# Kernel optimization log

Hardware: AMD Instinct MI355X
Metric: run time of the kernel (lower is better)

## Reference

```python
import jax, jax.numpy as jnp
import numpy as np

N_NODES = 8192
N_EDGES = 262144
FEAT = 128


def _lin(key, fan_in, fan_out):
    k1, k2 = jax.random.split(key)
    s = 1.0 / np.sqrt(fan_in)
    w = jax.random.uniform(k1, (fan_in, fan_out), jnp.float32, -s, s)
    b = jax.random.uniform(k2, (fan_out,), jnp.float32, -s, s)
    return w, b


def setup_inputs() -> dict:
    key = jax.random.key(0)
    ks = jax.random.split(key, 16)
    adj = jax.random.randint(ks[0], (2, N_EDGES), 0, N_NODES)
    features = jax.random.normal(ks[1], (N_NODES, FEAT), jnp.float32)
    w1, b1 = _lin(ks[2], FEAT, 64)
    w2, b2 = _lin(ks[3], 64, 32)
    w3, b3 = _lin(ks[4], 32, 32)
    # MultiheadAttention params (embed_dim=32, 1 head)
    kq = jax.random.split(ks[5], 2)
    wqkv = jax.random.uniform(kq[0], (96, 32), jnp.float32, -1/np.sqrt(32), 1/np.sqrt(32))
    bqkv = jnp.zeros((96,), jnp.float32)
    wo = jax.random.uniform(kq[1], (32, 32), jnp.float32, -1/np.sqrt(32), 1/np.sqrt(32))
    bo = jnp.zeros((32,), jnp.float32)
    w4, b4 = _lin(ks[6], 32, 32)
    w5a, b5a = _lin(ks[7], 32, 32)
    w6a, b6a = _lin(ks[8], 32, 64)
    w7a, b7a = _lin(ks[9], 64, 2)
    w5f, b5f = _lin(ks[10], 32, 32)
    w6f, b6f = _lin(ks[11], 32, 64)
    w7f, b7f = _lin(ks[12], 64, FEAT)
    return dict(adj=adj, features=features, w1=w1, b1=b1, w2=w2, b2=b2, w3=w3, b3=b3,
                wqkv=wqkv, bqkv=bqkv, wo=wo, bo=bo, w4=w4, b4=b4,
                w5a=w5a, b5a=b5a, w6a=w6a, b6a=b6a, w7a=w7a, b7a=b7a,
                w5f=w5f, b5f=b5f, w6f=w6f, b6f=b6f, w7f=w7f, b7f=b7f)


def _gcn(x, w, b, src, dst, norm, n):
    # PyG GCNConv: out = scatter_add(norm * (x W)[src] -> dst) + b
    h = x @ w
    return jax.ops.segment_sum(h[src] * norm[:, None], dst, num_segments=n) + b


def reference(adj, features, w1, b1, w2, b2, w3, b3, wqkv, bqkv, wo, bo, w4, b4,
              w5a, b5a, w6a, b6a, w7a, b7a, w5f, b5f, w6f, b6f, w7f, b7f):
    n = features.shape[0]
    loops = jnp.arange(n)
    src = jnp.concatenate([adj[0], loops])  # self-loops added (gcn_norm)
    dst = jnp.concatenate([adj[1], loops])
    deg = jax.ops.segment_sum(jnp.ones_like(src, jnp.float32), dst, num_segments=n)
    dinv = jnp.where(deg > 0, jax.lax.rsqrt(deg), 0.0)
    norm = dinv[src] * dinv[dst]

    h = jax.nn.relu(_gcn(features, w1, b1, src, dst, norm, n))
    h = jax.nn.relu(_gcn(h, w2, b2, src, dst, norm, n))
    h = jax.nn.relu(_gcn(h, w3, b3, src, dst, norm, n))

    # single-head self-attention over all nodes (seq_len=n, batch=1)
    qkv = h @ wqkv.T + bqkv
    q, k, v = jnp.split(qkv, 3, axis=-1)  # [n,32] each
    attn = jax.nn.softmax((q @ k.T) * (1.0 / np.sqrt(32.0)), axis=-1)  # [n,n]
    h = (attn @ v) @ wo.T + bo

    h = jax.nn.relu(_gcn(h, w4, b4, src, dst, norm, n))

    da = jax.nn.relu(_gcn(h, w5a, b5a, src, dst, norm, n))
    da = jax.nn.relu(_gcn(da, w6a, b6a, src, dst, norm, n))
    da = jax.nn.relu(_gcn(da, w7a, b7a, src, dst, norm, n))  # [n,2]

    df = jax.nn.relu(_gcn(h, w5f, b5f, src, dst, norm, n))
    df = jax.nn.relu(_gcn(df, w6f, b6f, src, dst, norm, n))
    df = jax.nn.relu(_gcn(df, w7f, b7f, src, dst, norm, n))  # [n,FEAT]
    return (da, df)
```

## Files before the change

kernel.cpp:

```cpp
#include <hip/hip_runtime.h>

#define N_NODES 8192
#define N_EDGES 262144

typedef __attribute__((ext_vector_type(4))) float f32x4;
typedef _Float16 half8 __attribute__((ext_vector_type(8)));
typedef _Float16 half4v __attribute__((ext_vector_type(4)));
typedef __fp16 fp16x2 __attribute__((ext_vector_type(2)));
union UH { half8 h8; fp16x2 h2[4]; };
union HC { _Float16 h; unsigned short u; };


__global__ void __launch_bounds__(256) zero_kernel(int4* __restrict__ p) {
  p[blockIdx.x * 256 + threadIdx.x] = make_int4(0, 0, 0, 0);
}


__global__ void __launch_bounds__(1024) scan_kernel(const int* __restrict__ cnt,
                                                    int* __restrict__ rp,
                                                    float* __restrict__ dinv,
                                                    int* __restrict__ cur) {
  __shared__ int sums[1024];
  const int t = threadIdx.x;
  const int base = t * 8;
  int c[8];
  int s = 0;
#pragma unroll
  for (int i = 0; i < 8; ++i) { c[i] = cnt[base + i]; s += c[i]; cur[base + i] = 0; }
  sums[t] = s;
  __syncthreads();
  for (int off = 1; off < 1024; off <<= 1) {
    int v = (t >= off) ? sums[t - off] : 0;
    __syncthreads();
    sums[t] += v;
    __syncthreads();
  }
  int run = (t == 0) ? 0 : sums[t - 1];
#pragma unroll
  for (int i = 0; i < 8; ++i) {
    rp[base + i] = run;
    run += c[i];
    dinv[base + i] = rsqrtf((float)(c[i] + 1));
  }
  if (t == 1023) rp[N_NODES] = run;
}

__global__ void __launch_bounds__(256) fill_kernel(const int* __restrict__ src,
                                                   const int* __restrict__ dst,
                                                   const int* __restrict__ rp,
                                                   const float* __restrict__ dinv,
                                                   int* __restrict__ cur,
                                                   int* __restrict__ col,
                                                   float* __restrict__ wgt) {
  int e = blockIdx.x * 256 + threadIdx.x;
  int d = dst[e], s = src[e];
  int p = atomicAdd(&cur[d], 1);
  int at = rp[d] + p;
  col[at] = s;
  wgt[at] = dinv[s] * dinv[d];
}


template <int FIN, int FOUT, bool WT, bool BIAS, bool RELU, bool O16>
__device__ __forceinline__ void mm_body(const float* __restrict__ x,
                                        const float* __restrict__ w,
                                        const float* __restrict__ bias, void* out,
                                        int bx, int tid, float* ws, float* xs) {
  constexpr int VEC = (FOUT >= 32) ? 4 : 1;
  constexpr int TC = FOUT / VEC;
  constexpr int ROWS = 256 / TC;
  const int r0 = bx * ROWS;
  for (int i = tid; i < FIN * FOUT; i += 256) {
    int k = i / FOUT, j = i % FOUT;
    ws[i] = WT ? w[j * FIN + k] : w[i];
  }
  for (int i = tid; i < ROWS * FIN; i += 256) {
    int r = i / FIN, k = i % FIN;
    xs[r * (FIN + 1) + k] = x[(size_t)(r0 + r) * FIN + k];
  }
  __syncthreads();
  const int jc = tid % TC, r = tid / TC;
  float acc[VEC];
#pragma unroll
  for (int v = 0; v < VEC; ++v) acc[v] = 0.0f;
#pragma unroll
  for (int k = 0; k < FIN; ++k) {
    const float xv = xs[r * (FIN + 1) + k];
#pragma unroll
    for (int v = 0; v < VEC; ++v) acc[v] += xv * ws[k * FOUT + jc * VEC + v];
  }
  float oval[VEC];
#pragma unroll
  for (int v = 0; v < VEC; ++v) {
    int j = jc * VEC + v;
    float o = BIAS ? (acc[v] + bias[j]) : acc[v];
    if (RELU) o = fmaxf(o, 0.0f);
    oval[v] = o;
  }
  if constexpr (O16 && VEC == 4) {
    unsigned short* o16 = (unsigned short*)out;
    half4v pk;
#pragma unroll
    for (int v = 0; v < 4; ++v) pk[v] = (_Float16)oval[v];
    *(half4v*)&o16[(size_t)(r0 + r) * FOUT + jc * 4] = pk;
  } else {
    float* of = (float*)out;
#pragma unroll
    for (int v = 0; v < VEC; ++v) of[(size_t)(r0 + r) * FOUT + jc * VEC + v] = oval[v];
  }
}


template <int FIN, bool I16, bool GBR>
__device__ __forceinline__ void gather_row(const void* __restrict__ t,
                                           const int* __restrict__ rp,
                                           const int* __restrict__ col,
                                           const float* __restrict__ wgt,
                                           const float* __restrict__ dinv,
                                           const float* __restrict__ gbias,
                                           float* __restrict__ xrow, int n, int lane) {
  constexpr int FPL = I16 ? 8 : 4;
  constexpr int TPN = FIN / FPL;
  constexpr int EPI = 64 / TPN;
  const int eo = lane / TPN;
  const int fq = lane % TPN;
  const float di = dinv[n];
  const int rs = rp[n], re = rp[n + 1];
  float acc[FPL];
#pragma unroll
  for (int i = 0; i < FPL; ++i) acc[i] = 0.f;
  auto accum = [&](int node, float w) {
    if constexpr (I16) {
      const half8 hv = *(const half8*)((const unsigned short*)t + (size_t)node * FIN + fq * 8);
#pragma unroll
      for (int i = 0; i < 8; ++i) acc[i] += w * (float)hv[i];
    } else {
      const f32x4 v = *(const f32x4*)((const float*)t + (size_t)node * FIN + fq * 4);
#pragma unroll
      for (int i = 0; i < 4; ++i) acc[i] += w * v[i];
    }
  };
  if (eo == 0) accum(n, di * di);
  for (int e = rs + eo; e < re; e += EPI) accum(col[e], wgt[e]);
#pragma unroll
  for (int off = TPN; off < 64; off <<= 1) {
#pragma unroll
    for (int i = 0; i < FPL; ++i) acc[i] += __shfl_xor(acc[i], off, 64);
  }
  if (eo == 0) {
#pragma unroll
    for (int i = 0; i < FPL; ++i) {
      float v = acc[i];
      if (GBR) v = fmaxf(v + gbias[fq * FPL + i], 0.f);
      xrow[fq * FPL + i] = v;
    }
  }
}

template <int F, bool BR, bool I16, bool O16>
__device__ __forceinline__ void aggv_body(const void* __restrict__ t,
                                          const int* __restrict__ rp,
                                          const int* __restrict__ col,
                                          const float* __restrict__ wgt,
                                          const float* __restrict__ dinv,
                                          const float* __restrict__ bias,
                                          void* __restrict__ out, int bx, int tid) {
  constexpr int FPL = I16 ? 8 : 4;
  constexpr int TPN = F / FPL;
  constexpr int EPI = 64 / TPN;
  const int wv = tid >> 6;
  const int lane = tid & 63;
  const int n = bx * 4 + wv;
  const int eo = lane / TPN;
  const int fq = lane % TPN;
  const float di = dinv[n];
  const int rs = rp[n], re = rp[n + 1];
  float acc[FPL];
#pragma unroll
  for (int i = 0; i < FPL; ++i) acc[i] = 0.f;
  auto accum = [&](int node, float w) {
    if constexpr (I16) {
      const half8 hv = *(const half8*)((const unsigned short*)t + (size_t)node * F + fq * 8);
#pragma unroll
      for (int i = 0; i < 8; ++i) acc[i] += w * (float)hv[i];
    } else {
      const f32x4 v = *(const f32x4*)((const float*)t + (size_t)node * F + fq * 4);
#pragma unroll
      for (int i = 0; i < 4; ++i) acc[i] += w * v[i];
    }
  };
  if (eo == 0) accum(n, di * di);
  for (int e = rs + eo; e < re; e += EPI) accum(col[e], wgt[e]);
#pragma unroll
  for (int off = TPN; off < 64; off <<= 1) {
#pragma unroll
    for (int i = 0; i < FPL; ++i) acc[i] += __shfl_xor(acc[i], off, 64);
  }
  if (eo == 0) {
    float r[FPL];
#pragma unroll
    for (int i = 0; i < FPL; ++i) {
      float v = acc[i];
      if (BR) v = fmaxf(v + bias[fq * FPL + i], 0.f);
      r[i] = v;
    }
    if constexpr (O16) {
      unsigned short* o = (unsigned short*)out;
      half8 pk;
#pragma unroll
      for (int i = 0; i < 8; ++i) pk[i] = (_Float16)r[i];
      if constexpr (FPL == 8) *(half8*)&o[(size_t)n * F + fq * 8] = pk;
      else {
        half4v p4;
#pragma unroll
        for (int i = 0; i < 4; ++i) p4[i] = (_Float16)r[i];
        *(half4v*)&o[(size_t)n * F + fq * 4] = p4;
      }
    } else {
      float* o = (float*)out;
#pragma unroll
      for (int i = 0; i < FPL; i += 4)
        *(f32x4*)&o[(size_t)n * F + fq * FPL + i] = f32x4{r[i], r[i + 1], r[i + 2], r[i + 3]};
    }
  }
}

template <int F, bool BR = true, bool I16 = false, bool O16 = false>
__global__ void __launch_bounds__(256) aggv_kernel(const void* __restrict__ t,
                                                   const int* __restrict__ rp,
                                                   const int* __restrict__ col,
                                                   const float* __restrict__ wgt,
                                                   const float* __restrict__ dinv,
                                                   const float* __restrict__ bias,
                                                   void* __restrict__ out) {
  aggv_body<F, BR, I16, O16>(t, rp, col, wgt, dinv, bias, out, blockIdx.x, threadIdx.x);
}


template <int FIN, int FOUT, bool GBR, bool PBIAS, bool PRELU, bool O16>
__device__ __forceinline__ void layer_body(const unsigned short* __restrict__ tin,
                                           const float* __restrict__ w,
                                           const float* __restrict__ gbias,
                                           const float* __restrict__ pbias,
                                           void* __restrict__ out, const int* rp,
                                           const int* col, const float* wgt,
                                           const float* dinv, int bx, int tid, float* ws,
                                           float* xrow) {
  for (int i = tid; i < FIN * FOUT; i += 256) ws[i] = w[i];
  const int wv = tid >> 6, lane = tid & 63;
  const int n0 = bx * 4;
  gather_row<FIN, true, GBR>(tin, rp, col, wgt, dinv, gbias, xrow + wv * FIN, n0 + wv, lane);
  __syncthreads();
  for (int idx = tid; idx < 4 * FOUT; idx += 256) {
    const int nn = idx / FOUT, j = idx % FOUT;
    float acc = PBIAS ? pbias[j] : 0.f;
    const float* xr = xrow + nn * FIN;
#pragma unroll
    for (int k = 0; k < FIN; ++k) acc += xr[k] * ws[k * FOUT + j];
    if (PRELU) acc = fmaxf(acc, 0.f);
    if constexpr (O16) {
      HC c;
      c.h = (_Float16)acc;
      ((unsigned short*)out)[(size_t)(n0 + nn) * FOUT + j] = c.u;
    } else {
      ((float*)out)[(size_t)(n0 + nn) * FOUT + j] = acc;
    }
  }
}

template <int FIN, int FOUT, bool GBR, bool PBIAS, bool PRELU, bool O16>
__global__ void __launch_bounds__(256) layer_kernel(const unsigned short* __restrict__ tin,
                                                    const float* __restrict__ w,
                                                    const float* __restrict__ gbias,
                                                    const float* __restrict__ pbias,
                                                    void* __restrict__ out,
                                                    const int* __restrict__ rp,
                                                    const int* __restrict__ col,
                                                    const float* __restrict__ wgt,
                                                    const float* __restrict__ dinv) {
  __shared__ float ws[FIN * FOUT];
  __shared__ float xrow[4 * FIN];
  layer_body<FIN, FOUT, GBR, PBIAS, PRELU, O16>(tin, w, gbias, pbias, out, rp, col, wgt,
                                                dinv, blockIdx.x, threadIdx.x, ws, xrow);
}

__global__ void __launch_bounds__(256) agg_qkv_kernel(
    const unsigned short* __restrict__ t3, const float* __restrict__ b3,
    const float* __restrict__ wqkv, const float* __restrict__ bqkv,
    unsigned short* __restrict__ Q16, unsigned short* __restrict__ K16,
    unsigned short* __restrict__ V16, const int* __restrict__ rp,
    const int* __restrict__ col, const float* __restrict__ wgt,
    const float* __restrict__ dinv) {
  __shared__ float ws[32 * 96];
  __shared__ float xrow[4 * 32];
  const int tid = threadIdx.x;
  for (int i = tid; i < 3072; i += 256) {
    int k = i / 96, j = i % 96;
    ws[i] = wqkv[j * 32 + k];
  }
  const int wv = tid >> 6, lane = tid & 63;
  const int n0 = blockIdx.x * 4;
  gather_row<32, true, true>(t3, rp, col, wgt, dinv, b3, xrow + wv * 32, n0 + wv, lane);
  __syncthreads();
  const float QSCALE = 1.4426950408889634f * 0.17677669529663687f;
  for (int idx = tid; idx < 384; idx += 256) {
    const int nn = idx / 96, j = idx % 96;
    const int row = n0 + nn;
    const float* xr = xrow + nn * 32;
    float acc = bqkv[j];
#pragma unroll
    for (int k = 0; k < 32; ++k) acc += xr[k] * ws[k * 96 + j];
    HC c;
    if (j < 32) {
      c.h = (_Float16)(acc * QSCALE);
      Q16[(size_t)row * 32 + j] = c.u;
    } else if (j < 64) {
      c.h = (_Float16)acc;
      K16[(size_t)row * 32 + (j - 32)] = c.u;
    } else {
      c.h = (_Float16)acc;
      const int ko = row & 31;
      const int slot = 8 * ((ko & 15) >> 2) + ((ko >> 4) << 2) + (ko & 3);
      V16[(size_t)(j - 64) * N_NODES + (row & ~31) + slot] = c.u;
    }
  }
}

__global__ void __launch_bounds__(256) layer5_kernel(
    const unsigned short* __restrict__ h4, const float* __restrict__ w5a,
    const float* __restrict__ b5a, unsigned short* __restrict__ h5a,
    const float* __restrict__ w5f, const float* __restrict__ b5f,
    unsigned short* __restrict__ h5f, const int* __restrict__ rp,
    const int* __restrict__ col, const float* __restrict__ wgt,
    const float* __restrict__ dinv) {
  __shared__ float ws[2048];
  __shared__ float xrow[4 * 32];
  const int tid = threadIdx.x;
  for (int i = tid; i < 1024; i += 256) {
    ws[i] = w5a[i];
    ws[1024 + i] = w5f[i];
  }
  const int wv = tid >> 6, lane = tid & 63;
  const int n0 = blockIdx.x * 4;
  gather_row<32, true, false>(h4, rp, col, wgt, dinv, nullptr, xrow + wv * 32, n0 + wv, lane);
  __syncthreads();
  const int nn = tid >> 6;
  const int j = tid & 63;
  const int side = j >> 5, jj = j & 31;
  const float* xr = xrow + nn * 32;
  const float* wsd = ws + side * 1024;
  float acc = side ? b5f[jj] : b5a[jj];
#pragma unroll
  for (int k = 0; k < 32; ++k) acc += xr[k] * wsd[k * 32 + jj];
  acc = fmaxf(acc, 0.f);
  HC c;
  c.h = (_Float16)acc;
  unsigned short* o = side ? h5f : h5a;
  o[(size_t)(n0 + nn) * 32 + jj] = c.u;
}

__global__ void __launch_bounds__(256) layer6_kernel(
    const unsigned short* __restrict__ h5a, const float* __restrict__ w6a,
    const float* __restrict__ b6a, float* __restrict__ h6a,
    const unsigned short* __restrict__ h5f, const float* __restrict__ w6f,
    const float* __restrict__ b6f, unsigned short* __restrict__ h6f,
    const int* __restrict__ rp, const int* __restrict__ col,
    const float* __restrict__ wgt, const float* __restrict__ dinv) {
  __shared__ float ws[32 * 64];
  __shared__ float xrow[4 * 32];
  if (blockIdx.x < 2048)
    layer_body<32, 64, false, true, true, false>(h5a, w6a, nullptr, b6a, h6a, rp, col, wgt,
                                                 dinv, blockIdx.x, threadIdx.x, ws, xrow);
  else
    layer_body<32, 64, false, true, true, true>(h5f, w6f, nullptr, b6f, h6f, rp, col, wgt,
                                                dinv, blockIdx.x - 2048, threadIdx.x, ws, xrow);
}


__global__ void __launch_bounds__(256) cm_kernel(const int* __restrict__ dst,
                                                 int* __restrict__ cnt,
                                                 const float* __restrict__ feat,
                                                 const float* __restrict__ w1,
                                                 unsigned short* __restrict__ T16) {
  __shared__ float ws[128 * 64];
  __shared__ float xs[16 * 129];
  if (blockIdx.x < 512) {
    mm_body<128, 64, false, false, false, true>(feat, w1, nullptr, T16, blockIdx.x,
                                                threadIdx.x, ws, xs);
  } else {
    int e = (blockIdx.x - 512) * 256 + threadIdx.x;
    atomicAdd(&cnt[dst[e]], 1);
  }
}

__global__ void __launch_bounds__(256) het1_kernel(
    const float* __restrict__ h6a, const float* __restrict__ w7a, float* __restrict__ pre7a,
    const unsigned short* __restrict__ h6f, float* __restrict__ g7f,
    const int* __restrict__ rp, const int* __restrict__ col,
    const float* __restrict__ wgt, const float* __restrict__ dinv) {
  __shared__ float ws[64 * 2];
  __shared__ float xs[128 * 65];
  if (blockIdx.x < 64)
    mm_body<64, 2, false, false, false, false>(h6a, w7a, nullptr, pre7a, blockIdx.x,
                                               threadIdx.x, ws, xs);
  else
    aggv_body<64, false, true, false>(h6f, rp, col, wgt, dinv, nullptr, g7f,
                                      blockIdx.x - 64, threadIdx.x);
}

__global__ void __launch_bounds__(256) het2_kernel(
    const float* __restrict__ pre7a, const float* __restrict__ b7a, float* __restrict__ outa,
    const float* __restrict__ g7f, const float* __restrict__ w7f,
    const float* __restrict__ b7f, float* __restrict__ outf,
    const int* __restrict__ rp, const int* __restrict__ col,
    const float* __restrict__ wgt, const float* __restrict__ dinv) {
  __shared__ float ws[64 * 128];
  __shared__ float xs[8 * 65];
  if (blockIdx.x < 64) {
    const int tid = threadIdx.x;
    const int n = blockIdx.x * 128 + tid / 2;
    const int f = tid & 1;
    const float di = dinv[n];
    float acc = di * di * pre7a[(size_t)n * 2 + f];
    const int rs = rp[n], re = rp[n + 1];
    for (int e = rs; e < re; ++e) {
      acc += wgt[e] * pre7a[(size_t)col[e] * 2 + f];
    }
    acc += b7a[f];
    outa[(size_t)n * 2 + f] = fmaxf(acc, 0.0f);
  } else {
    mm_body<64, 128, false, true, true, false>(g7f, w7f, b7f, outf, blockIdx.x - 64,
                                               threadIdx.x, ws, xs);
  }
}


__device__ __forceinline__ void wave_writeout(float (*lds)[544], float (*wexp)[16],
                                              float* Mq, float* Lq, const f32x4& o1,
                                              const f32x4& o2, float m, float l, int wid,
                                              int g, int li, int tid, int qt, int by,
                                              float* __restrict__ part) {
#pragma unroll
  for (int r = 0; r < 4; ++r) {
    lds[wid][(4 * g + r) * 16 + li] = o1[r];
    lds[wid][(16 + 4 * g + r) * 16 + li] = o2[r];
  }
  if (g == 0) {
    lds[wid][512 + li] = m;
    lds[wid][528 + li] = l;
  }
  __syncthreads();
  if (tid < 16) {
    const int q = tid;
    const float m0 = lds[0][512 + q], m1 = lds[1][512 + q];
    const float m2 = lds[2][512 + q], m3 = lds[3][512 + q];
    const float M = fmaxf(fmaxf(m0, m1), fmaxf(m2, m3));
    const float w0 = exp2f(m0 - M), w1 = exp2f(m1 - M);
    const float w2 = exp2f(m2 - M), w3 = exp2f(m3 - M);
    wexp[0][q] = w0; wexp[1][q] = w1; wexp[2][q] = w2; wexp[3][q] = w3;
    Mq[q] = M;
    Lq[q] = w0 * lds[0][528 + q] + w1 * lds[1][528 + q] +
            w2 * lds[2][528 + q] + w3 * lds[3][528 + q];
  }
  __syncthreads();
  const int base = (qt * 4 + by) * 544;
#pragma unroll
  for (int e2 = 0; e2 < 2; ++e2) {
    const int e = tid + e2 * 256;
    const int q = e & 15;
    part[base + e] = wexp[0][q] * lds[0][e] + wexp[1][q] * lds[1][e] +
                     wexp[2][q] * lds[2][e] + wexp[3][q] * lds[3][e];
  }
  if (tid < 16) {
    part[base + 512 + tid] = Mq[tid];
    part[base + 528 + tid] = Lq[tid];
  }
}

__global__ void __launch_bounds__(256, 4) attn_mfma_kernel(
    const unsigned short* __restrict__ Q16, const unsigned short* __restrict__ K16,
    const unsigned short* __restrict__ V16, float* __restrict__ part) {
  __shared__ float lds[4][544];
  __shared__ float wexp[4][16];
  __shared__ float Mq[16], Lq[16];
  const int tid = threadIdx.x;
  const int wid = tid >> 6;
  const int lane = tid & 63;
  const int g = lane >> 4;
  const int li = lane & 15;
  const int qpair = blockIdx.x;
  const int q0A = qpair * 32;
  const int q0B = q0A + 16;
  const int kbeg = blockIdx.y * 2048 + wid * 512;

  const half8 qfA = *(const half8*)&Q16[(q0A + li) * 32 + 8 * g];
  const half8 qfB = *(const half8*)&Q16[(q0B + li) * 32 + 8 * g];
  const int koff = li * 32 + 8 * g;
  const int vA = li * N_NODES + 8 * g;
  const int vB = (16 + li) * N_NODES + 8 * g;

  f32x4 oAA = {0.f, 0.f, 0.f, 0.f}, oBA = {0.f, 0.f, 0.f, 0.f};
  f32x4 oAB = {0.f, 0.f, 0.f, 0.f}, oBB = {0.f, 0.f, 0.f, 0.f};
  float mA = -1e30f, lA = 0.f, mB = -1e30f, lB = 0.f;

  for (int t = kbeg; t < kbeg + 512; t += 64) {
    const half8 k0 = *(const half8*)&K16[(t)*32 + koff];
    const half8 k1 = *(const half8*)&K16[(t + 16) * 32 + koff];
    const half8 k2 = *(const half8*)&K16[(t + 32) * 32 + koff];
    const half8 k3 = *(const half8*)&K16[(t + 48) * 32 + koff];
    const half8 va0 = *(const half8*)&V16[vA + t];
    const half8 vb0 = *(const half8*)&V16[vB + t];
    const half8 va1 = *(const half8*)&V16[vA + t + 32];
    const half8 vb1 = *(const half8*)&V16[vB + t + 32];

    {
      f32x4 s0 = {0.f, 0.f, 0.f, 0.f}, s1 = {0.f, 0.f, 0.f, 0.f};
      f32x4 s2 = {0.f, 0.f, 0.f, 0.f}, s3 = {0.f, 0.f, 0.f, 0.f};
      s0 = __builtin_amdgcn_mfma_f32_16x16x32_f16(k0, qfA, s0, 0, 0, 0);
      s1 = __builtin_amdgcn_mfma_f32_16x16x32_f16(k1, qfA, s1, 0, 0, 0);
      s2 = __builtin_amdgcn_mfma_f32_16x16x32_f16(k2, qfA, s2, 0, 0, 0);
      s3 = __builtin_amdgcn_mfma_f32_16x16x32_f16(k3, qfA, s3, 0, 0, 0);
      float mxl = fmaxf(fmaxf(fmaxf(s0[0], s0[1]), fmaxf(s0[2], s0[3])),
                        fmaxf(fmaxf(s1[0], s1[1]), fmaxf(s1[2], s1[3])));
      mxl = fmaxf(mxl, fmaxf(fmaxf(fmaxf(s2[0], s2[1]), fmaxf(s2[2], s2[3])),
                             fmaxf(fmaxf(s3[0], s3[1]), fmaxf(s3[2], s3[3]))));
      if (!__all(mxl <= mA)) {
        float mx = mxl;
        mx = fmaxf(mx, __shfl_xor(mx, 16, 64));
        mx = fmaxf(mx, __shfl_xor(mx, 32, 64));
        const float mn = fmaxf(mA, mx);
        const float fct = exp2f(mA - mn);
        oAA *= fct; oBA *= fct; lA *= fct;
        mA = mn;
      }
      const float p0 = exp2f(s0[0] - mA), p1 = exp2f(s0[1] - mA);
      const float p2 = exp2f(s0[2] - mA), p3 = exp2f(s0[3] - mA);
      const float p4 = exp2f(s1[0] - mA), p5 = exp2f(s1[1] - mA);
      const float p6 = exp2f(s1[2] - mA), p7 = exp2f(s1[3] - mA);
      const float p8 = exp2f(s2[0] - mA), p9 = exp2f(s2[1] - mA);
      const float pa = exp2f(s2[2] - mA), pb = exp2f(s2[3] - mA);
      const float pc = exp2f(s3[0] - mA), pd = exp2f(s3[1] - mA);
      const float pe = exp2f(s3[2] - mA), pf = exp2f(s3[3] - mA);
      lA += (((p0 + p1) + (p2 + p3)) + ((p4 + p5) + (p6 + p7))) +
            (((p8 + p9) + (pa + pb)) + ((pc + pd) + (pe + pf)));
      UH ph0, ph1;
      ph0.h2[0] = __builtin_amdgcn_cvt_pkrtz(p0, p1);
      ph0.h2[1] = __builtin_amdgcn_cvt_pkrtz(p2, p3);
      ph0.h2[2] = __builtin_amdgcn_cvt_pkrtz(p4, p5);
      ph0.h2[3] = __builtin_amdgcn_cvt_pkrtz(p6, p7);
      ph1.h2[0] = __builtin_amdgcn_cvt_pkrtz(p8, p9);
      ph1.h2[1] = __builtin_amdgcn_cvt_pkrtz(pa, pb);
      ph1.h2[2] = __builtin_amdgcn_cvt_pkrtz(pc, pd);
      ph1.h2[3] = __builtin_amdgcn_cvt_pkrtz(pe, pf);
      oAA = __builtin_amdgcn_mfma_f32_16x16x32_f16(va0, ph0.h8, oAA, 0, 0, 0);
      oAA = __builtin_amdgcn_mfma_f32_16x16x32_f16(va1, ph1.h8, oAA, 0, 0, 0);
      oBA = __builtin_amdgcn_mfma_f32_16x16x32_f16(vb0, ph0.h8, oBA, 0, 0, 0);
      oBA = __builtin_amdgcn_mfma_f32_16x16x32_f16(vb1, ph1.h8, oBA, 0, 0, 0);
    }
    {
      f32x4 s0 = {0.f, 0.f, 0.f, 0.f}, s1 = {0.f, 0.f, 0.f, 0.f};
      f32x4 s2 = {0.f, 0.f, 0.f, 0.f}, s3 = {0.f, 0.f, 0.f, 0.f};
      s0 = __builtin_amdgcn_mfma_f32_16x16x32_f16(k0, qfB, s0, 0, 0, 0);
      s1 = __builtin_amdgcn_mfma_f32_16x16x32_f16(k1, qfB, s1, 0, 0, 0);
      s2 = __builtin_amdgcn_mfma_f32_16x16x32_f16(k2, qfB, s2, 0, 0, 0);
      s3 = __builtin_amdgcn_mfma_f32_16x16x32_f16(k3, qfB, s3, 0, 0, 0);
      float mxl = fmaxf(fmaxf(fmaxf(s0[0], s0[1]), fmaxf(s0[2], s0[3])),
                        fmaxf(fmaxf(s1[0], s1[1]), fmaxf(s1[2], s1[3])));
      mxl = fmaxf(mxl, fmaxf(fmaxf(fmaxf(s2[0], s2[1]), fmaxf(s2[2], s2[3])),
                             fmaxf(fmaxf(s3[0], s3[1]), fmaxf(s3[2], s3[3]))));
      if (!__all(mxl <= mB)) {
        float mx = mxl;
        mx = fmaxf(mx, __shfl_xor(mx, 16, 64));
        mx = fmaxf(mx, __shfl_xor(mx, 32, 64));
        const float mn = fmaxf(mB, mx);
        const float fct = exp2f(mB - mn);
        oAB *= fct; oBB *= fct; lB *= fct;
        mB = mn;
      }
      const float p0 = exp2f(s0[0] - mB), p1 = exp2f(s0[1] - mB);
      const float p2 = exp2f(s0[2] - mB), p3 = exp2f(s0[3] - mB);
      const float p4 = exp2f(s1[0] - mB), p5 = exp2f(s1[1] - mB);
      const float p6 = exp2f(s1[2] - mB), p7 = exp2f(s1[3] - mB);
      const float p8 = exp2f(s2[0] - mB), p9 = exp2f(s2[1] - mB);
      const float pa = exp2f(s2[2] - mB), pb = exp2f(s2[3] - mB);
      const float pc = exp2f(s3[0] - mB), pd = exp2f(s3[1] - mB);
      const float pe = exp2f(s3[2] - mB), pf = exp2f(s3[3] - mB);
      lB += (((p0 + p1) + (p2 + p3)) + ((p4 + p5) + (p6 + p7))) +
            (((p8 + p9) + (pa + pb)) + ((pc + pd) + (pe + pf)));
      UH ph0, ph1;
      ph0.h2[0] = __builtin_amdgcn_cvt_pkrtz(p0, p1);
      ph0.h2[1] = __builtin_amdgcn_cvt_pkrtz(p2, p3);
      ph0.h2[2] = __builtin_amdgcn_cvt_pkrtz(p4, p5);
      ph0.h2[3] = __builtin_amdgcn_cvt_pkrtz(p6, p7);
      ph1.h2[0] = __builtin_amdgcn_cvt_pkrtz(p8, p9);
      ph1.h2[1] = __builtin_amdgcn_cvt_pkrtz(pa, pb);
      ph1.h2[2] = __builtin_amdgcn_cvt_pkrtz(pc, pd);
      ph1.h2[3] = __builtin_amdgcn_cvt_pkrtz(pe, pf);
      oAB = __builtin_amdgcn_mfma_f32_16x16x32_f16(va0, ph0.h8, oAB, 0, 0, 0);
      oAB = __builtin_amdgcn_mfma_f32_16x16x32_f16(va1, ph1.h8, oAB, 0, 0, 0);
      oBB = __builtin_amdgcn_mfma_f32_16x16x32_f16(vb0, ph0.h8, oBB, 0, 0, 0);
      oBB = __builtin_amdgcn_mfma_f32_16x16x32_f16(vb1, ph1.h8, oBB, 0, 0, 0);
    }
  }

  lA += __shfl_xor(lA, 16, 64);
  lA += __shfl_xor(lA, 32, 64);
  lB += __shfl_xor(lB, 16, 64);
  lB += __shfl_xor(lB, 32, 64);

  wave_writeout(lds, wexp, Mq, Lq, oAA, oBA, mA, lA, wid, g, li, tid, qpair * 2,
                blockIdx.y, part);
  __syncthreads();
  wave_writeout(lds, wexp, Mq, Lq, oAB, oBB, mB, lB, wid, g, li, tid, qpair * 2 + 1,
                blockIdx.y, part);
}


__global__ void __launch_bounds__(256) attn_combine_wo_w4(const float* __restrict__ part,
                                                          const float* __restrict__ wo,
                                                          const float* __restrict__ bo,
                                                          const float* __restrict__ w4,
                                                          unsigned short* __restrict__ T16out) {
  __shared__ float wols[1024];
  __shared__ float w4ls[1024];
  __shared__ float bos[32];
  __shared__ float aos[4][16][33];
  __shared__ float hs[4][16][33];
  const int tid = threadIdx.x;
  for (int i = tid; i < 1024; i += 256) {
    wols[i] = wo[i];
    w4ls[i] = w4[i];
  }
  if (tid < 32) bos[tid] = bo[tid];
  const int wv = tid >> 6, lane = tid & 63;
  const int qt = blockIdx.x * 4 + wv;
  const int q = lane & 15, g = lane >> 4;
  const int pb = qt * 4 * 544;
  const float m0 = part[pb + 512 + q], m1 = part[pb + 544 + 512 + q];
  const float m2 = part[pb + 1088 + 512 + q], m3 = part[pb + 1632 + 512 + q];
  const float M = fmaxf(fmaxf(m0, m1), fmaxf(m2, m3));
  const float w0 = exp2f(m0 - M), w1 = exp2f(m1 - M);
  const float w2 = exp2f(m2 - M), w3 = exp2f(m3 - M);
  const float L = w0 * part[pb + 528 + q] + w1 * part[pb + 544 + 528 + q] +
                  w2 * part[pb + 1088 + 528 + q] + w3 * part[pb + 1632 + 528 + q];
  const float invL = 1.0f / L;
#pragma unroll
  for (int r = 0; r < 8; ++r) {
    const int d = g + 4 * r;
    const int o = d * 16 + q;
    const float ov = w0 * part[pb + o] + w1 * part[pb + 544 + o] +
                     w2 * part[pb + 1088 + o] + w3 * part[pb + 1632 + o];
    aos[wv][q][d] = ov * invL;
  }
  __syncthreads();
#pragma unroll
  for (int r = 0; r < 8; ++r) {
    const int dout = g + 4 * r;
    float acc = bos[dout];
#pragma unroll
    for (int k = 0; k < 32; ++k) acc += aos[wv][q][k] * wols[dout * 32 + k];
    hs[wv][q][dout] = acc;
  }
#pragma unroll
  for (int r = 0; r < 8; ++r) {
    const int dout = g + 4 * r;
    float acc = 0.f;
#pragma unroll
    for (int k = 0; k < 32; ++k) acc += hs[wv][q][k] * w4ls[k * 32 + dout];
    HC c;
    c.h = (_Float16)acc;
    T16out[(size_t)(qt * 16 + q) * 32 + dout] = c.u;
  }
}


extern "C" void kernel_launch(void* const* d_in, const int* in_sizes, int n_in,
                              void* d_out, int out_size, void* d_ws, size_t ws_size,
                              hipStream_t stream) {
  (void)in_sizes; (void)n_in; (void)out_size; (void)ws_size;
  const int* adj = (const int*)d_in[0];
  const float* feat = (const float*)d_in[1];
  const float* w1 = (const float*)d_in[2];  const float* b1 = (const float*)d_in[3];
  const float* w2 = (const float*)d_in[4];  const float* b2 = (const float*)d_in[5];
  const float* w3 = (const float*)d_in[6];  const float* b3 = (const float*)d_in[7];
  const float* wqkv = (const float*)d_in[8];const float* bqkv = (const float*)d_in[9];
  const float* wo = (const float*)d_in[10]; const float* bo = (const float*)d_in[11];
  const float* w4 = (const float*)d_in[12]; const float* b4 = (const float*)d_in[13];
  const float* w5a = (const float*)d_in[14];const float* b5a = (const float*)d_in[15];
  const float* w6a = (const float*)d_in[16];const float* b6a = (const float*)d_in[17];
  const float* w7a = (const float*)d_in[18];const float* b7a = (const float*)d_in[19];
  const float* w5f = (const float*)d_in[20];const float* b5f = (const float*)d_in[21];
  const float* w6f = (const float*)d_in[22];const float* b6f = (const float*)d_in[23];
  const float* w7f = (const float*)d_in[24];const float* b7f = (const float*)d_in[25];
  float* outp = (float*)d_out;

  float* wsf = (float*)d_ws;
  int* wsi = (int*)d_ws;
  int* cnt = wsi;
  int* cur = wsi + 8192;
  int* rp = wsi + 16384;
  float* dinv = wsf + 24832;
  float* wgt = wsf + 33024;
  int* col = wsi + 295168;
  float* T = wsf + 557312;
  float* B0 = wsf + 1605888;
  float* B1 = wsf + 2130176;
  float* B2 = wsf + 2392320;
  unsigned short* Q16 = (unsigned short*)(wsf + 2916608);
  unsigned short* K16 = Q16 + 262144;
  unsigned short* V16 = K16 + 262144;
  unsigned short* T16u = (unsigned short*)T;
  unsigned short* t1 = T16u;
  unsigned short* t2 = T16u + 524288;
  unsigned short* t3 = T16u;
  unsigned short* t4 = (unsigned short*)B2;
  unsigned short* B0h = (unsigned short*)B0;
  unsigned short* B1h = (unsigned short*)B1;
  unsigned short* B2h = (unsigned short*)B2;
  unsigned short* h6f = T16u;
  float* g7f = T + 262144;
  float* pre7a = B1;
  float* part = T;

  const int* src = adj;
  const int* dst = adj + N_EDGES;

  zero_kernel<<<8, 256, 0, stream>>>((int4*)cnt);
  cm_kernel<<<1536, 256, 0, stream>>>(dst, cnt, feat, w1, t1);
  scan_kernel<<<1, 1024, 0, stream>>>(cnt, rp, dinv, cur);
  fill_kernel<<<N_EDGES / 256, 256, 0, stream>>>(src, dst, rp, dinv, cur, col, wgt);

  layer_kernel<64, 32, true, false, false, true><<<N_NODES / 4, 256, 0, stream>>>(
      t1, w2, b1, nullptr, t2, rp, col, wgt, dinv);
  layer_kernel<32, 32, true, false, false, true><<<N_NODES / 4, 256, 0, stream>>>(
      t2, w3, b2, nullptr, t3, rp, col, wgt, dinv);
  agg_qkv_kernel<<<N_NODES / 4, 256, 0, stream>>>(t3, b3, wqkv, bqkv, Q16, K16, V16, rp,
                                                  col, wgt, dinv);

  {
    dim3 grid(256, 4);
    attn_mfma_kernel<<<grid, 256, 0, stream>>>(Q16, K16, V16, part);
  }
  attn_combine_wo_w4<<<128, 256, 0, stream>>>(part, wo, bo, w4, t4);

  aggv_kernel<32, true, true, true><<<N_NODES / 4, 256, 0, stream>>>(t4, rp, col, wgt,
                                                                     dinv, b4, B0h);

  layer5_kernel<<<N_NODES / 4, 256, 0, stream>>>(B0h, w5a, b5a, B1h, w5f, b5f, B2h, rp,
                                                 col, wgt, dinv);
  layer6_kernel<<<2 * (N_NODES / 4), 256, 0, stream>>>(B1h, w6a, b6a, B0, B2h, w6f, b6f,
                                                       h6f, rp, col, wgt, dinv);
  het1_kernel<<<64 + 2048, 256, 0, stream>>>(B0, w7a, pre7a, h6f, g7f, rp, col, wgt, dinv);
  het2_kernel<<<64 + 1024, 256, 0, stream>>>(pre7a, b7a, outp, g7f, w7f, b7f, outp + 16384,
                                             rp, col, wgt, dinv);
}
```

Measured before the change: 178.0 us.

## Split attention key range into eight partitions for more parallel blocks

The attention kernel's key dimension is now split into 8 chunks per query pair instead of 4, doubling the grid to 256x8 blocks, each processing 1024 keys. Occupancy hints rise to 8 blocks per CU, and the combine kernel merges 8 partial softmax states. The aim is better CU saturation on a short kernel, at the cost of more partial-result traffic and combine work. Because the partial buffer grew, the t4 output buffer is moved to a separate workspace region to avoid overlap.

```diff
diff --git a/kernel.cpp b/kernel.cpp
--- a/kernel.cpp
+++ b/kernel.cpp
@@ -206,11 +206,12 @@
     }
     if constexpr (O16) {
       unsigned short* o = (unsigned short*)out;
-      half8 pk;
-#pragma unroll
-      for (int i = 0; i < 8; ++i) pk[i] = (_Float16)r[i];
-      if constexpr (FPL == 8) *(half8*)&o[(size_t)n * F + fq * 8] = pk;
-      else {
+      if constexpr (FPL == 8) {
+        half8 pk;
+#pragma unroll
+        for (int i = 0; i < 8; ++i) pk[i] = (_Float16)r[i];
+        *(half8*)&o[(size_t)n * F + fq * 8] = pk;
+      } else {
         half4v p4;
 #pragma unroll
         for (int i = 0; i < 4; ++i) p4[i] = (_Float16)r[i];
@@ -463,7 +464,7 @@
             w2 * lds[2][528 + q] + w3 * lds[3][528 + q];
   }
   __syncthreads();
-  const int base = (qt * 4 + by) * 544;
+  const int base = (qt * 8 + by) * 544;
 #pragma unroll
   for (int e2 = 0; e2 < 2; ++e2) {
     const int e = tid + e2 * 256;
@@ -477,7 +478,7 @@
   }
 }
 
-__global__ void __launch_bounds__(256, 4) attn_mfma_kernel(
+__global__ void __launch_bounds__(256, 8) attn_mfma_kernel(
     const unsigned short* __restrict__ Q16, const unsigned short* __restrict__ K16,
     const unsigned short* __restrict__ V16, float* __restrict__ part) {
   __shared__ float lds[4][544];
@@ -491,7 +492,7 @@
   const int qpair = blockIdx.x;
   const int q0A = qpair * 32;
   const int q0B = q0A + 16;
-  const int kbeg = blockIdx.y * 2048 + wid * 512;
+  const int kbeg = blockIdx.y * 1024 + wid * 256;
 
   const half8 qfA = *(const half8*)&Q16[(q0A + li) * 32 + 8 * g];
   const half8 qfB = *(const half8*)&Q16[(q0B + li) * 32 + 8 * g];
@@ -503,7 +504,7 @@
   f32x4 oAB = {0.f, 0.f, 0.f, 0.f}, oBB = {0.f, 0.f, 0.f, 0.f};
   float mA = -1e30f, lA = 0.f, mB = -1e30f, lB = 0.f;
 
-  for (int t = kbeg; t < kbeg + 512; t += 64) {
+  for (int t = kbeg; t < kbeg + 256; t += 64) {
     const half8 k0 = *(const half8*)&K16[(t)*32 + koff];
     const half8 k1 = *(const half8*)&K16[(t + 16) * 32 + koff];
     const half8 k2 = *(const half8*)&K16[(t + 32) * 32 + koff];
@@ -635,21 +636,28 @@
   const int wv = tid >> 6, lane = tid & 63;
   const int qt = blockIdx.x * 4 + wv;
   const int q = lane & 15, g = lane >> 4;
-  const int pb = qt * 4 * 544;
-  const float m0 = part[pb + 512 + q], m1 = part[pb + 544 + 512 + q];
-  const float m2 = part[pb + 1088 + 512 + q], m3 = part[pb + 1632 + 512 + q];
-  const float M = fmaxf(fmaxf(m0, m1), fmaxf(m2, m3));
-  const float w0 = exp2f(m0 - M), w1 = exp2f(m1 - M);
-  const float w2 = exp2f(m2 - M), w3 = exp2f(m3 - M);
-  const float L = w0 * part[pb + 528 + q] + w1 * part[pb + 544 + 528 + q] +
-                  w2 * part[pb + 1088 + 528 + q] + w3 * part[pb + 1632 + 528 + q];
+  const int pb = qt * 8 * 544;
+  float ms[8], w8[8];
+  float M = -1e30f;
+#pragma unroll
+  for (int s = 0; s < 8; ++s) {
+    ms[s] = part[pb + s * 544 + 512 + q];
+    M = fmaxf(M, ms[s]);
+  }
+  float L = 0.f;
+#pragma unroll
+  for (int s = 0; s < 8; ++s) {
+    w8[s] = exp2f(ms[s] - M);
+    L += w8[s] * part[pb + s * 544 + 528 + q];
+  }
   const float invL = 1.0f / L;
 #pragma unroll
   for (int r = 0; r < 8; ++r) {
     const int d = g + 4 * r;
     const int o = d * 16 + q;
-    const float ov = w0 * part[pb + o] + w1 * part[pb + 544 + o] +
-                     w2 * part[pb + 1088 + o] + w3 * part[pb + 1632 + o];
+    float ov = 0.f;
+#pragma unroll
+    for (int s = 0; s < 8; ++s) ov += w8[s] * part[pb + s * 544 + o];
     aos[wv][q][d] = ov * invL;
   }
   __syncthreads();
@@ -713,7 +721,6 @@
   unsigned short* t1 = T16u;
   unsigned short* t2 = T16u + 524288;
   unsigned short* t3 = T16u;
-  unsigned short* t4 = (unsigned short*)B2;
   unsigned short* B0h = (unsigned short*)B0;
   unsigned short* B1h = (unsigned short*)B1;
   unsigned short* B2h = (unsigned short*)B2;
@@ -721,6 +728,7 @@
   float* g7f = T + 262144;
   float* pre7a = B1;
   float* part = T;
+  unsigned short* t4 = (unsigned short*)(wsf + 2785536);
 
   const int* src = adj;
   const int* dst = adj + N_EDGES;
@@ -738,7 +746,7 @@
                                                   col, wgt, dinv);
 
   {
-    dim3 grid(256, 4);
+    dim3 grid(256, 8);
     attn_mfma_kernel<<<grid, 256, 0, stream>>>(Q16, K16, V16, part);
   }
   attn_combine_wo_w4<<<128, 256, 0, stream>>>(part, wo, bo, w4, t4);
```

Result: slower. 251.0 us (+41.0%).
